# Kernel tuning notes

Measured on AMD Instinct MI355X. Metric: run time of the kernel, lower is better.

The kernel has to match this reference:

```python
import jax, jax.numpy as jnp
import numpy as np

N_NODES = 50000
N_EDGES = 1600000
IN_CH = 128
EDGE_DIM = 32
OUT_CH = 128


def setup_inputs() -> dict:
    key = jax.random.key(0)
    ks = jax.random.split(key, 6)
    x = jax.random.normal(ks[0], (N_NODES, IN_CH), dtype=jnp.float32)
    row = jax.random.randint(ks[1], (N_EDGES,), 0, N_NODES, dtype=jnp.int32)
    col = jax.random.randint(ks[2], (N_EDGES,), 0, N_NODES, dtype=jnp.int32)
    norm = jax.random.uniform(ks[3], (N_EDGES,), dtype=jnp.float32)
    edge_attr = jax.random.normal(ks[4], (N_EDGES, EDGE_DIM), dtype=jnp.float32)
    # glorot init for lin.weight (shape [in+edge, out] stored transposed vs torch)
    fan = IN_CH + EDGE_DIM + OUT_CH
    std = jnp.sqrt(6.0 / fan)
    W = jax.random.uniform(ks[5], (IN_CH + EDGE_DIM, OUT_CH), dtype=jnp.float32,
                           minval=-std, maxval=std)
    b = jnp.zeros((OUT_CH,), dtype=jnp.float32)
    return {"x": x, "row": row, "col": col, "norm": norm,
            "edge_attr": edge_attr, "W": W, "b": b}


def reference(x, row, col, norm, edge_attr, W, b):
    # graph @ x : for each edge e=(row[e], col[e], norm[e]),
    # out[row] += norm * x[col]  (sparse normalized-adjacency spmm)
    msg_x = norm[:, None] * x[col]                      # [E, IN_CH]
    agg = jax.ops.segment_sum(msg_x, row, num_segments=N_NODES)  # [N, IN_CH]
    # edge-feature messages scattered to source rows
    msg_e = norm[:, None] * edge_attr                   # [E, EDGE_DIM]
    agg_e = jax.ops.segment_sum(msg_e, row, num_segments=N_NODES)  # [N, EDGE_DIM]
    out = jnp.concatenate([agg, agg_e], axis=1)         # [N, IN_CH+EDGE_DIM]
    return out @ W + b
```

## Files before the change

### kernel.cpp

```cpp
#include <hip/hip_runtime.h>

#define N_NODES  50000
#define N_EDGES  1600000
#define IN_CH    128
#define EDGE_DIM 32
#define AGG_DIM  160
#define OUT_CH   128
#define CAP      96
#define SCAN_BS  1024
#define NBLK     ((N_NODES + SCAN_BS - 1) / SCAN_BS)

typedef float f32x4 __attribute__((ext_vector_type(4)));
typedef float f32x2 __attribute__((ext_vector_type(2)));
typedef int   i32x4 __attribute__((ext_vector_type(4)));
typedef unsigned int u32x4 __attribute__((ext_vector_type(4)));
typedef unsigned int       uint32;
typedef unsigned long long uint64;
typedef unsigned short     ushort16;

__device__ __forceinline__ uint32 bf16rn(float f) {
    const uint32 u = __float_as_uint(f);
    return (u + 0x7FFFu + ((u >> 16) & 1u)) >> 16;
}

__global__ __launch_bounds__(256) void prep_kernel(
    const float* __restrict__ x, const int* __restrict__ row,
    const int* __restrict__ col, const float* __restrict__ norm,
    int* __restrict__ cnt, i32x4* __restrict__ csr, ushort16* __restrict__ xq)
{
    const int i = blockIdx.x * 256 + threadIdx.x;
    const f32x4 v = ((const f32x4*)x)[i];
    uint2 u;
    u.x = bf16rn(v.x) | (bf16rn(v.y) << 16);
    u.y = bf16rn(v.z) | (bf16rn(v.w) << 16);
    ((uint2*)xq)[i] = u;
    const int r   = row[i];
    const int pos = atomicAdd(&cnt[r], 1);
    if (pos < CAP) {
        i32x4 p;
        p.x = col[i]; p.y = __float_as_int(norm[i]); p.z = i; p.w = 0;
        csr[(size_t)r * CAP + pos] = p;
    }
}

__global__ __launch_bounds__(256) void gather_gemm_a_kernel(
    const ushort16* __restrict__ xq,
    const i32x4*    __restrict__ csr,
    const float*    __restrict__ ea,
    const int*      __restrict__ cnt,
    const float*    __restrict__ W,
    const float*    __restrict__ b,
    float*          __restrict__ out)
{
    __shared__ float aggS[4][AGG_DIM];
    __shared__ f32x2 part[4][4][64];
    const int w    = threadIdx.x >> 6;
    const int lane = threadIdx.x & 63;
    const int q    = lane >> 4;
    const int ql   = lane & 15;
    const int n    = blockIdx.x * 4 + w;

    const int start = n * CAP;
    const int deg   = cnt[n];
    const int end   = start + ((deg < CAP) ? deg : CAP);

    float ax[8] = {0, 0, 0, 0, 0, 0, 0, 0};
    float ae0 = 0.f, ae1 = 0.f;

    int e = start;

    i32x4 r0, r1, r2, r3;
    if (e + 16 <= end) {
        r0 = __builtin_nontemporal_load(csr + e + q);
        r1 = __builtin_nontemporal_load(csr + e + 4 + q);
        r2 = __builtin_nontemporal_load(csr + e + 8 + q);
        r3 = __builtin_nontemporal_load(csr + e + 12 + q);
    }
    while (e + 16 <= end) {
        const u32x4 x0 = ((const u32x4*)(xq + (size_t)r0.x * IN_CH))[ql];
        const u32x4 x1 = ((const u32x4*)(xq + (size_t)r1.x * IN_CH))[ql];
        const u32x4 x2 = ((const u32x4*)(xq + (size_t)r2.x * IN_CH))[ql];
        const u32x4 x3 = ((const u32x4*)(xq + (size_t)r3.x * IN_CH))[ql];
        const f32x2 e0 = __builtin_nontemporal_load(
            (const f32x2*)(ea + (size_t)r0.z * EDGE_DIM) + ql);
        const f32x2 e1 = __builtin_nontemporal_load(
            (const f32x2*)(ea + (size_t)r1.z * EDGE_DIM) + ql);
        const f32x2 e2 = __builtin_nontemporal_load(
            (const f32x2*)(ea + (size_t)r2.z * EDGE_DIM) + ql);
        const f32x2 e3 = __builtin_nontemporal_load(
            (const f32x2*)(ea + (size_t)r3.z * EDGE_DIM) + ql);
        const float n0 = __int_as_float(r0.y);
        const float n1 = __int_as_float(r1.y);
        const float n2 = __int_as_float(r2.y);
        const float n3 = __int_as_float(r3.y);
        e += 16;
        r0 = __builtin_nontemporal_load(csr + e + q);
        r1 = __builtin_nontemporal_load(csr + e + 4 + q);
        r2 = __builtin_nontemporal_load(csr + e + 8 + q);
        r3 = __builtin_nontemporal_load(csr + e + 12 + q);

        #pragma unroll
        for (int j = 0; j < 4; ++j) {
            ax[2*j]   = fmaf(n0, __uint_as_float(x0[j] << 16),         ax[2*j]);
            ax[2*j+1] = fmaf(n0, __uint_as_float(x0[j] & 0xffff0000u), ax[2*j+1]);
            ax[2*j]   = fmaf(n1, __uint_as_float(x1[j] << 16),         ax[2*j]);
            ax[2*j+1] = fmaf(n1, __uint_as_float(x1[j] & 0xffff0000u), ax[2*j+1]);
            ax[2*j]   = fmaf(n2, __uint_as_float(x2[j] << 16),         ax[2*j]);
            ax[2*j+1] = fmaf(n2, __uint_as_float(x2[j] & 0xffff0000u), ax[2*j+1]);
            ax[2*j]   = fmaf(n3, __uint_as_float(x3[j] << 16),         ax[2*j]);
            ax[2*j+1] = fmaf(n3, __uint_as_float(x3[j] & 0xffff0000u), ax[2*j+1]);
        }
        ae0 = fmaf(n0, e0.x, ae0);  ae1 = fmaf(n0, e0.y, ae1);
        ae0 = fmaf(n1, e1.x, ae0);  ae1 = fmaf(n1, e1.y, ae1);
        ae0 = fmaf(n2, e2.x, ae0);  ae1 = fmaf(n2, e2.y, ae1);
        ae0 = fmaf(n3, e3.x, ae0);  ae1 = fmaf(n3, e3.y, ae1);
    }

    for (; e + 8 <= end; e += 8) {
        const int sA = e + q;
        const int sB = e + 4 + q;
        const i32x4 pA = __builtin_nontemporal_load(csr + sA);
        const i32x4 pB = __builtin_nontemporal_load(csr + sB);
        const float nA = __int_as_float(pA.y);
        const float nB = __int_as_float(pB.y);
        const u32x4 xA = ((const u32x4*)(xq + (size_t)pA.x * IN_CH))[ql];
        const u32x4 xB = ((const u32x4*)(xq + (size_t)pB.x * IN_CH))[ql];
        const f32x2 eA = __builtin_nontemporal_load(
            (const f32x2*)(ea + (size_t)pA.z * EDGE_DIM) + ql);
        const f32x2 eB = __builtin_nontemporal_load(
            (const f32x2*)(ea + (size_t)pB.z * EDGE_DIM) + ql);

        #pragma unroll
        for (int j = 0; j < 4; ++j) {
            ax[2*j]   = fmaf(nA, __uint_as_float(xA[j] << 16),         ax[2*j]);
            ax[2*j+1] = fmaf(nA, __uint_as_float(xA[j] & 0xffff0000u), ax[2*j+1]);
            ax[2*j]   = fmaf(nB, __uint_as_float(xB[j] << 16),         ax[2*j]);
            ax[2*j+1] = fmaf(nB, __uint_as_float(xB[j] & 0xffff0000u), ax[2*j+1]);
        }
        ae0 = fmaf(nA, eA.x, ae0);
        ae1 = fmaf(nA, eA.y, ae1);
        ae0 = fmaf(nB, eB.x, ae0);
        ae1 = fmaf(nB, eB.y, ae1);
    }

    if (e < end) {
        const int sA = e + q;
        if (sA < end) {
            const i32x4 pA = __builtin_nontemporal_load(csr + sA);
            const float nA = __int_as_float(pA.y);
            const u32x4 xA = ((const u32x4*)(xq + (size_t)pA.x * IN_CH))[ql];
            const f32x2 eA = __builtin_nontemporal_load(
                (const f32x2*)(ea + (size_t)pA.z * EDGE_DIM) + ql);
            #pragma unroll
            for (int j = 0; j < 4; ++j) {
                ax[2*j]   = fmaf(nA, __uint_as_float(xA[j] << 16),         ax[2*j]);
                ax[2*j+1] = fmaf(nA, __uint_as_float(xA[j] & 0xffff0000u), ax[2*j+1]);
            }
            ae0 = fmaf(nA, eA.x, ae0);
            ae1 = fmaf(nA, eA.y, ae1);
        }
        const int sB = e + 4 + q;
        if (sB < end) {
            const i32x4 pB = __builtin_nontemporal_load(csr + sB);
            const float nB = __int_as_float(pB.y);
            const u32x4 xB = ((const u32x4*)(xq + (size_t)pB.x * IN_CH))[ql];
            const f32x2 eB = __builtin_nontemporal_load(
                (const f32x2*)(ea + (size_t)pB.z * EDGE_DIM) + ql);
            #pragma unroll
            for (int j = 0; j < 4; ++j) {
                ax[2*j]   = fmaf(nB, __uint_as_float(xB[j] << 16),         ax[2*j]);
                ax[2*j+1] = fmaf(nB, __uint_as_float(xB[j] & 0xffff0000u), ax[2*j+1]);
            }
            ae0 = fmaf(nB, eB.x, ae0);
            ae1 = fmaf(nB, eB.y, ae1);
        }
    }

    #pragma unroll
    for (int j = 0; j < 8; ++j) {
        ax[j] += __shfl_xor(ax[j], 16, 64);
        ax[j] += __shfl_xor(ax[j], 32, 64);
    }
    ae0 += __shfl_xor(ae0, 16, 64); ae0 += __shfl_xor(ae0, 32, 64);
    ae1 += __shfl_xor(ae1, 16, 64); ae1 += __shfl_xor(ae1, 32, 64);

    if (lane < 16) {
        const f32x4 v0 = {ax[0], ax[1], ax[2], ax[3]};
        const f32x4 v1 = {ax[4], ax[5], ax[6], ax[7]};
        ((f32x4*)aggS[w])[2 * ql]     = v0;
        ((f32x4*)aggS[w])[2 * ql + 1] = v1;
        aggS[w][IN_CH + 2 * ql]       = ae0;
        aggS[w][IN_CH + 2 * ql + 1]   = ae1;
    }
    __syncthreads();

    f32x2 pacc[4] = {{0.f, 0.f}, {0.f, 0.f}, {0.f, 0.f}, {0.f, 0.f}};
    const int k0 = 40 * w;
    for (int k = k0; k < k0 + 40; ++k) {
        const f32x2 wv = ((const f32x2*)(W + k * OUT_CH))[lane];
        #pragma unroll
        for (int m = 0; m < 4; ++m) {
            const float av = aggS[m][k];
            pacc[m].x = fmaf(av, wv.x, pacc[m].x);
            pacc[m].y = fmaf(av, wv.y, pacc[m].y);
        }
    }
    #pragma unroll
    for (int m = 0; m < 4; ++m) part[w][m][lane] = pacc[m];
    __syncthreads();

    const int m = w;
    f32x2 o = ((const f32x2*)b)[lane];
    #pragma unroll
    for (int w2 = 0; w2 < 4; ++w2) o += part[w2][m][lane];
    ((f32x2*)(out + (size_t)(blockIdx.x * 4 + m) * OUT_CH))[lane] = o;
}

__global__ __launch_bounds__(256) void hist_kernel(
    const int* __restrict__ row, int* __restrict__ counts)
{
    const int e = blockIdx.x * 256 + threadIdx.x;
    if (e < N_EDGES) atomicAdd(&counts[row[e]], 1);
}

__global__ __launch_bounds__(1024) void scan_local_kernel(
    const int* __restrict__ counts, int* __restrict__ ptr, int* __restrict__ bsums)
{
    __shared__ int waveTot[16];
    __shared__ int waveInc[16];
    const int tid  = threadIdx.x;
    const int lane = tid & 63;
    const int wid  = tid >> 6;
    const int i    = blockIdx.x * SCAN_BS + tid;
    const int v    = (i < N_NODES) ? counts[i] : 0;

    int s = v;
    #pragma unroll
    for (int off = 1; off < 64; off <<= 1) {
        const int t = __shfl_up(s, off, 64);
        if (lane >= off) s += t;
    }
    if (lane == 63) waveTot[wid] = s;
    __syncthreads();
    if (wid == 0) {
        int t = (lane < 16) ? waveTot[lane] : 0;
        #pragma unroll
        for (int off = 1; off < 16; off <<= 1) {
            const int u = __shfl_up(t, off, 64);
            if (lane >= off) t += u;
        }
        if (lane < 16) waveInc[lane] = t;
    }
    __syncthreads();
    const int excl = ((wid == 0) ? 0 : waveInc[wid - 1]) + s - v;
    if (i < N_NODES) ptr[i] = excl;
    if (tid == 0) bsums[blockIdx.x] = waveInc[15];
}

__global__ __launch_bounds__(64) void scan_sums_kernel(
    const int* __restrict__ bsums, int* __restrict__ boff)
{
    const int lane = threadIdx.x;
    const int v = (lane < NBLK) ? bsums[lane] : 0;
    int s = v;
    #pragma unroll
    for (int off = 1; off < 64; off <<= 1) {
        const int t = __shfl_up(s, off, 64);
        if (lane >= off) s += t;
    }
    if (lane < NBLK) boff[lane] = s - v;
}

__global__ __launch_bounds__(256) void scan_add_kernel(
    int* __restrict__ ptr, const int* __restrict__ boff)
{
    const int i = blockIdx.x * 256 + threadIdx.x;
    if (i < N_NODES) ptr[i] += boff[i >> 10];
}

__global__ __launch_bounds__(256) void csr_build_b_kernel(
    const int* __restrict__ row, const int* __restrict__ col,
    const float* __restrict__ norm, int* __restrict__ ptr, i32x4* __restrict__ csr)
{
    const int e = blockIdx.x * 256 + threadIdx.x;
    if (e >= N_EDGES) return;
    const int r   = row[e];
    const int pos = atomicAdd(&ptr[r], 1);
    i32x4 p;
    p.x = col[e]; p.y = __float_as_int(norm[e]); p.z = e; p.w = 0;
    csr[pos] = p;
}

__global__ __launch_bounds__(256) void gather_gemm_b_kernel(
    const float* __restrict__ x, const float* __restrict__ ea,
    const int* __restrict__ ptr, const i32x4* __restrict__ csr,
    const float* __restrict__ W, const float* __restrict__ b,
    float* __restrict__ out)
{
    __shared__ float aggS[4][AGG_DIM];
    const int w    = threadIdx.x >> 6;
    const int lane = threadIdx.x & 63;
    const int half = lane >> 5;
    const int hl   = lane & 31;
    const int n    = blockIdx.x * 4 + w;

    const int start = (n > 0) ? ptr[n - 1] : 0;
    const int end   = ptr[n];

    f32x4 accx = {0.f, 0.f, 0.f, 0.f};
    f32x4 acce = {0.f, 0.f, 0.f, 0.f};

    int e = start;
    for (; e + 4 <= end; e += 4) {
        const i32x4 pA = __builtin_nontemporal_load(&csr[e + half]);
        const i32x4 pB = __builtin_nontemporal_load(&csr[e + 2 + half]);
        const float nA = __int_as_float(pA.y);
        const float nB = __int_as_float(pB.y);
        const f32x4 xA = ((const f32x4*)(x + (size_t)pA.x * IN_CH))[hl];
        const f32x4 xB = ((const f32x4*)(x + (size_t)pB.x * IN_CH))[hl];
        accx += nA * xA;
        accx += nB * xB;
        if (hl < 8) {
            const f32x4 eA = __builtin_nontemporal_load((const f32x4*)(ea + (size_t)pA.z * EDGE_DIM) + hl);
            const f32x4 eB = __builtin_nontemporal_load((const f32x4*)(ea + (size_t)pB.z * EDGE_DIM) + hl);
            acce += nA * eA;
            acce += nB * eB;
        }
    }
    for (; e < end; e += 2) {
        const int eA = e + half;
        if (eA < end) {
            const i32x4 pA = __builtin_nontemporal_load(&csr[eA]);
            const float nA = __int_as_float(pA.y);
            const f32x4 xA = ((const f32x4*)(x + (size_t)pA.x * IN_CH))[hl];
            accx += nA * xA;
            if (hl < 8) {
                const f32x4 eAv = __builtin_nontemporal_load((const f32x4*)(ea + (size_t)pA.z * EDGE_DIM) + hl);
                acce += nA * eAv;
            }
        }
    }
    #pragma unroll
    for (int i = 0; i < 4; ++i) {
        accx[i] += __shfl_xor(accx[i], 32, 64);
        acce[i] += __shfl_xor(acce[i], 32, 64);
    }
    if (half == 0) {
        ((f32x4*)aggS[w])[hl] = accx;
        if (hl < 8) ((f32x4*)(aggS[w] + IN_CH))[hl] = acce;
    }
    __syncthreads();

    f32x2 acc = ((const f32x2*)b)[lane];
    #pragma unroll 8
    for (int k = 0; k < AGG_DIM; ++k) {
        const float av = aggS[w][k];
        const f32x2 wv = ((const f32x2*)(W + k * OUT_CH))[lane];
        acc.x += av * wv.x;
        acc.y += av * wv.y;
    }
    ((f32x2*)(out + (size_t)n * OUT_CH))[lane] = acc;
}

extern "C" void kernel_launch(void* const* d_in, const int* in_sizes, int n_in,
                              void* d_out, int out_size, void* d_ws, size_t ws_size,
                              hipStream_t stream)
{
    const float* x    = (const float*)d_in[0];
    const int*   row  = (const int*)  d_in[1];
    const int*   col  = (const int*)  d_in[2];
    const float* norm = (const float*)d_in[3];
    const float* ea   = (const float*)d_in[4];
    const float* W    = (const float*)d_in[5];
    const float* b    = (const float*)d_in[6];
    float*       out  = (float*)d_out;

    char* ws = (char*)d_ws;

    if (ws_size >= (96ull << 20)) {
        int*      cnt = (int*)ws;
        i32x4*    csr = (i32x4*)(ws + (1ull << 20));
        ushort16* xq  = (ushort16*)(ws + (79ull << 20));

        (void)hipMemsetAsync(cnt, 0, (size_t)N_NODES * sizeof(int), stream);
        prep_kernel<<<N_EDGES / 256, 256, 0, stream>>>(
            x, row, col, norm, cnt, csr, xq);
        gather_gemm_a_kernel<<<N_NODES / 4, 256, 0, stream>>>(
            xq, csr, ea, cnt, W, b, out);
    } else {
        int*   counts = (int*)(ws);
        int*   ptr    = (int*)(ws + (256 << 10));
        int*   bsums  = (int*)(ws + (512 << 10));
        int*   boff   = (int*)(ws + (768 << 10));
        i32x4* csr    = (i32x4*)(ws + (1ull << 20));

        (void)hipMemsetAsync(counts, 0, (size_t)N_NODES * sizeof(int), stream);
        hist_kernel<<<(N_EDGES + 255) / 256, 256, 0, stream>>>(row, counts);
        scan_local_kernel<<<NBLK, SCAN_BS, 0, stream>>>(counts, ptr, bsums);
        scan_sums_kernel<<<1, 64, 0, stream>>>(bsums, boff);
        scan_add_kernel<<<(N_NODES + 255) / 256, 256, 0, stream>>>(ptr, boff);
        csr_build_b_kernel<<<(N_EDGES + 255) / 256, 256, 0, stream>>>(
            row, col, norm, ptr, csr);
        gather_gemm_b_kernel<<<N_NODES / 4, 256, 0, stream>>>(
            x, ea, ptr, csr, W, b, out);
    }
}
```

Baseline: 486.3 us.

## Aggregate edge features via atomics in prep kernel and shrink CSR records to 8 bytes

Moves the norm-weighted edge_attr segment sum out of the per-node gather kernel into the edge-parallel prep kernel, which reads edge_attr coalesced and scatters into a zeroed agg_e buffer with float atomics. The CSR record drops the edge index and padding, becoming a packed 64-bit (col, norm) pair. This removes scattered edge_attr reads and halves CSR traffic, at the cost of many global float atomics and nondeterministic summation order.

```diff
diff --git a/kernel.cpp b/kernel.cpp
--- a/kernel.cpp
+++ b/kernel.cpp
@@ -26,27 +26,52 @@
 __global__ __launch_bounds__(256) void prep_kernel(
     const float* __restrict__ x, const int* __restrict__ row,
     const int* __restrict__ col, const float* __restrict__ norm,
-    int* __restrict__ cnt, i32x4* __restrict__ csr, ushort16* __restrict__ xq)
-{
-    const int i = blockIdx.x * 256 + threadIdx.x;
-    const f32x4 v = ((const f32x4*)x)[i];
+    const float* __restrict__ ea,
+    int* __restrict__ cnt, uint64* __restrict__ csr,
+    ushort16* __restrict__ xq, float* __restrict__ agg_e)
+{
+    __shared__ int   s_row[256];
+    __shared__ float s_norm[256];
+    const int tid = threadIdx.x;
+    const int g   = blockIdx.x * 256 + tid;
+
+    const f32x4 v = ((const f32x4*)x)[g];
     uint2 u;
     u.x = bf16rn(v.x) | (bf16rn(v.y) << 16);
     u.y = bf16rn(v.z) | (bf16rn(v.w) << 16);
-    ((uint2*)xq)[i] = u;
-    const int r   = row[i];
+    ((uint2*)xq)[g] = u;
+
+    const int   r  = row[g];
+    const float nv = norm[g];
+    s_row[tid]  = r;
+    s_norm[tid] = nv;
     const int pos = atomicAdd(&cnt[r], 1);
     if (pos < CAP) {
-        i32x4 p;
-        p.x = col[i]; p.y = __float_as_int(norm[i]); p.z = i; p.w = 0;
-        csr[(size_t)r * CAP + pos] = p;
+        const uint64 rec = ((uint64)__float_as_uint(nv) << 32) | (uint32)col[g];
+        csr[(size_t)r * CAP + pos] = rec;
+    }
+    __syncthreads();
+
+    const int ql   = tid & 15;
+    const int esub = tid >> 4;
+    const int base = blockIdx.x * 256;
+    #pragma unroll 4
+    for (int it = 0; it < 16; ++it) {
+        const int   le   = it * 16 + esub;
+        const int   eidx = base + le;
+        const f32x2 ev   = __builtin_nontemporal_load(
+            (const f32x2*)(ea + (size_t)eidx * EDGE_DIM) + ql);
+        const float nn   = s_norm[le];
+        float* dst = agg_e + (size_t)s_row[le] * EDGE_DIM + 2 * ql;
+        atomicAdd(dst,     nn * ev.x);
+        atomicAdd(dst + 1, nn * ev.y);
     }
 }
 
 __global__ __launch_bounds__(256) void gather_gemm_a_kernel(
     const ushort16* __restrict__ xq,
-    const i32x4*    __restrict__ csr,
-    const float*    __restrict__ ea,
+    const uint64*   __restrict__ csr,
+    const float*    __restrict__ agg_e,
     const int*      __restrict__ cnt,
     const float*    __restrict__ W,
     const float*    __restrict__ b,
@@ -65,11 +90,10 @@
     const int end   = start + ((deg < CAP) ? deg : CAP);
 
     float ax[8] = {0, 0, 0, 0, 0, 0, 0, 0};
-    float ae0 = 0.f, ae1 = 0.f;
 
     int e = start;
 
-    i32x4 r0, r1, r2, r3;
+    uint64 r0, r1, r2, r3;
     if (e + 16 <= end) {
         r0 = __builtin_nontemporal_load(csr + e + q);
         r1 = __builtin_nontemporal_load(csr + e + 4 + q);
@@ -77,22 +101,14 @@
         r3 = __builtin_nontemporal_load(csr + e + 12 + q);
     }
     while (e + 16 <= end) {
-        const u32x4 x0 = ((const u32x4*)(xq + (size_t)r0.x * IN_CH))[ql];
-        const u32x4 x1 = ((const u32x4*)(xq + (size_t)r1.x * IN_CH))[ql];
-        const u32x4 x2 = ((const u32x4*)(xq + (size_t)r2.x * IN_CH))[ql];
-        const u32x4 x3 = ((const u32x4*)(xq + (size_t)r3.x * IN_CH))[ql];
-        const f32x2 e0 = __builtin_nontemporal_load(
-            (const f32x2*)(ea + (size_t)r0.z * EDGE_DIM) + ql);
-        const f32x2 e1 = __builtin_nontemporal_load(
-            (const f32x2*)(ea + (size_t)r1.z * EDGE_DIM) + ql);
-        const f32x2 e2 = __builtin_nontemporal_load(
-            (const f32x2*)(ea + (size_t)r2.z * EDGE_DIM) + ql);
-        const f32x2 e3 = __builtin_nontemporal_load(
-            (const f32x2*)(ea + (size_t)r3.z * EDGE_DIM) + ql);
-        const float n0 = __int_as_float(r0.y);
-        const float n1 = __int_as_float(r1.y);
-        const float n2 = __int_as_float(r2.y);
-        const float n3 = __int_as_float(r3.y);
+        const u32x4 x0 = ((const u32x4*)(xq + (size_t)(uint32)r0 * IN_CH))[ql];
+        const u32x4 x1 = ((const u32x4*)(xq + (size_t)(uint32)r1 * IN_CH))[ql];
+        const u32x4 x2 = ((const u32x4*)(xq + (size_t)(uint32)r2 * IN_CH))[ql];
+        const u32x4 x3 = ((const u32x4*)(xq + (size_t)(uint32)r3 * IN_CH))[ql];
+        const float n0 = __uint_as_float((uint32)(r0 >> 32));
+        const float n1 = __uint_as_float((uint32)(r1 >> 32));
+        const float n2 = __uint_as_float((uint32)(r2 >> 32));
+        const float n3 = __uint_as_float((uint32)(r3 >> 32));
         e += 16;
         r0 = __builtin_nontemporal_load(csr + e + q);
         r1 = __builtin_nontemporal_load(csr + e + 4 + q);
@@ -110,26 +126,15 @@
             ax[2*j]   = fmaf(n3, __uint_as_float(x3[j] << 16),         ax[2*j]);
             ax[2*j+1] = fmaf(n3, __uint_as_float(x3[j] & 0xffff0000u), ax[2*j+1]);
         }
-        ae0 = fmaf(n0, e0.x, ae0);  ae1 = fmaf(n0, e0.y, ae1);
-        ae0 = fmaf(n1, e1.x, ae0);  ae1 = fmaf(n1, e1.y, ae1);
-        ae0 = fmaf(n2, e2.x, ae0);  ae1 = fmaf(n2, e2.y, ae1);
-        ae0 = fmaf(n3, e3.x, ae0);  ae1 = fmaf(n3, e3.y, ae1);
     }
 
     for (; e + 8 <= end; e += 8) {
-        const int sA = e + q;
-        const int sB = e + 4 + q;
-        const i32x4 pA = __builtin_nontemporal_load(csr + sA);
-        const i32x4 pB = __builtin_nontemporal_load(csr + sB);
-        const float nA = __int_as_float(pA.y);
-        const float nB = __int_as_float(pB.y);
-        const u32x4 xA = ((const u32x4*)(xq + (size_t)pA.x * IN_CH))[ql];
-        const u32x4 xB = ((const u32x4*)(xq + (size_t)pB.x * IN_CH))[ql];
-        const f32x2 eA = __builtin_nontemporal_load(
-            (const f32x2*)(ea + (size_t)pA.z * EDGE_DIM) + ql);
-        const f32x2 eB = __builtin_nontemporal_load(
-            (const f32x2*)(ea + (size_t)pB.z * EDGE_DIM) + ql);
-
+        const uint64 pA = __builtin_nontemporal_load(csr + e + q);
+        const uint64 pB = __builtin_nontemporal_load(csr + e + 4 + q);
+        const float  nA = __uint_as_float((uint32)(pA >> 32));
+        const float  nB = __uint_as_float((uint32)(pB >> 32));
+        const u32x4  xA = ((const u32x4*)(xq + (size_t)(uint32)pA * IN_CH))[ql];
+        const u32x4  xB = ((const u32x4*)(xq + (size_t)(uint32)pB * IN_CH))[ql];
         #pragma unroll
         for (int j = 0; j < 4; ++j) {
             ax[2*j]   = fmaf(nA, __uint_as_float(xA[j] << 16),         ax[2*j]);
@@ -137,42 +142,30 @@
             ax[2*j]   = fmaf(nB, __uint_as_float(xB[j] << 16),         ax[2*j]);
             ax[2*j+1] = fmaf(nB, __uint_as_float(xB[j] & 0xffff0000u), ax[2*j+1]);
         }
-        ae0 = fmaf(nA, eA.x, ae0);
-        ae1 = fmaf(nA, eA.y, ae1);
-        ae0 = fmaf(nB, eB.x, ae0);
-        ae1 = fmaf(nB, eB.y, ae1);
     }
 
     if (e < end) {
         const int sA = e + q;
         if (sA < end) {
-            const i32x4 pA = __builtin_nontemporal_load(csr + sA);
-            const float nA = __int_as_float(pA.y);
-            const u32x4 xA = ((const u32x4*)(xq + (size_t)pA.x * IN_CH))[ql];
-            const f32x2 eA = __builtin_nontemporal_load(
-                (const f32x2*)(ea + (size_t)pA.z * EDGE_DIM) + ql);
+            const uint64 pA = __builtin_nontemporal_load(csr + sA);
+            const float  nA = __uint_as_float((uint32)(pA >> 32));
+            const u32x4  xA = ((const u32x4*)(xq + (size_t)(uint32)pA * IN_CH))[ql];
             #pragma unroll
             for (int j = 0; j < 4; ++j) {
                 ax[2*j]   = fmaf(nA, __uint_as_float(xA[j] << 16),         ax[2*j]);
                 ax[2*j+1] = fmaf(nA, __uint_as_float(xA[j] & 0xffff0000u), ax[2*j+1]);
             }
-            ae0 = fmaf(nA, eA.x, ae0);
-            ae1 = fmaf(nA, eA.y, ae1);
         }
         const int sB = e + 4 + q;
         if (sB < end) {
-            const i32x4 pB = __builtin_nontemporal_load(csr + sB);
-            const float nB = __int_as_float(pB.y);
-            const u32x4 xB = ((const u32x4*)(xq + (size_t)pB.x * IN_CH))[ql];
-            const f32x2 eB = __builtin_nontemporal_load(
-                (const f32x2*)(ea + (size_t)pB.z * EDGE_DIM) + ql);
+            const uint64 pB = __builtin_nontemporal_load(csr + sB);
+            const float  nB = __uint_as_float((uint32)(pB >> 32));
+            const u32x4  xB = ((const u32x4*)(xq + (size_t)(uint32)pB * IN_CH))[ql];
             #pragma unroll
             for (int j = 0; j < 4; ++j) {
                 ax[2*j]   = fmaf(nB, __uint_as_float(xB[j] << 16),         ax[2*j]);
                 ax[2*j+1] = fmaf(nB, __uint_as_float(xB[j] & 0xffff0000u), ax[2*j+1]);
             }
-            ae0 = fmaf(nB, eB.x, ae0);
-            ae1 = fmaf(nB, eB.y, ae1);
         }
     }
 
@@ -181,16 +174,15 @@
         ax[j] += __shfl_xor(ax[j], 16, 64);
         ax[j] += __shfl_xor(ax[j], 32, 64);
     }
-    ae0 += __shfl_xor(ae0, 16, 64); ae0 += __shfl_xor(ae0, 32, 64);
-    ae1 += __shfl_xor(ae1, 16, 64); ae1 += __shfl_xor(ae1, 32, 64);
 
     if (lane < 16) {
         const f32x4 v0 = {ax[0], ax[1], ax[2], ax[3]};
         const f32x4 v1 = {ax[4], ax[5], ax[6], ax[7]};
         ((f32x4*)aggS[w])[2 * ql]     = v0;
         ((f32x4*)aggS[w])[2 * ql + 1] = v1;
-        aggS[w][IN_CH + 2 * ql]       = ae0;
-        aggS[w][IN_CH + 2 * ql + 1]   = ae1;
+        const f32x2 ge = ((const f32x2*)(agg_e + (size_t)n * EDGE_DIM))[ql];
+        aggS[w][IN_CH + 2 * ql]     = ge.x;
+        aggS[w][IN_CH + 2 * ql + 1] = ge.y;
     }
     __syncthreads();
 
@@ -377,16 +369,19 @@
 
     char* ws = (char*)d_ws;
 
-    if (ws_size >= (96ull << 20)) {
-        int*      cnt = (int*)ws;
-        i32x4*    csr = (i32x4*)(ws + (1ull << 20));
-        ushort16* xq  = (ushort16*)(ws + (79ull << 20));
-
-        (void)hipMemsetAsync(cnt, 0, (size_t)N_NODES * sizeof(int), stream);
+    if (ws_size >= (64ull << 20)) {
+        int*      cnt   = (int*)ws;
+        float*    agg_e = (float*)(ws + (256 << 10));
+        uint64*   csr   = (uint64*)(ws + (7ull << 20));
+        ushort16* xq    = (ushort16*)(ws + (46ull << 20));
+
+        (void)hipMemsetAsync(ws, 0,
+            (size_t)(256 << 10) + (size_t)N_NODES * EDGE_DIM * sizeof(float),
+            stream);
         prep_kernel<<<N_EDGES / 256, 256, 0, stream>>>(
-            x, row, col, norm, cnt, csr, xq);
+            x, row, col, norm, ea, cnt, csr, xq, agg_e);
         gather_gemm_a_kernel<<<N_NODES / 4, 256, 0, stream>>>(
-            xq, csr, ea, cnt, W, b, out);
+            xq, csr, agg_e, cnt, W, b, out);
     } else {
         int*   counts = (int*)(ws);
         int*   ptr    = (int*)(ws + (256 << 10));
```

Result: slower. 749.1 us (+54.1%).
